# Optimization experiments

Measured on AMD Instinct MI355X. Metric: run time of the kernel, lower is better.

Reference implementation:

```python
import jax, jax.numpy as jnp
import numpy as np

B, N, D = 4, 4096, 512

def setup_inputs() -> dict:
    key = jax.random.key(0)
    ks = jax.random.split(key, 7)
    s = 1.0 / np.sqrt(D)
    return {
        "inputdata": jax.random.normal(ks[0], (B, N, D), dtype=jnp.float32),
        "Wq": jax.random.uniform(ks[1], (D, D), jnp.float32, -s, s),
        "bq": jax.random.uniform(ks[2], (D,), jnp.float32, -s, s),
        "Wk": jax.random.uniform(ks[3], (D, D), jnp.float32, -s, s),
        "bk": jax.random.uniform(ks[4], (D,), jnp.float32, -s, s),
        "Wv": jax.random.uniform(ks[5], (D, D), jnp.float32, -s, s),
        "bv": jax.random.uniform(ks[6], (D,), jnp.float32, -s, s),
    }

def reference(inputdata, Wq, bq, Wk, bk, Wv, bv):
    # torch nn.Linear: y = x @ W^T + b
    Q = jnp.einsum("bnd,ed->bne", inputdata, Wq) + bq  # [B,N,D]
    K = jnp.einsum("bnd,ed->bne", inputdata, Wk) + bk
    V = jnp.einsum("bnd,ed->bne", inputdata, Wv) + bv
    scores = jnp.einsum("bqd,bkd->bqk", Q, K)          # [B,N,N], no 1/sqrt(d) scale
    # NOTE: softmax over dim=1 (the QUERY axis), matching the original torch code
    attn = jax.nn.softmax(scores, axis=1)
    return jnp.einsum("bqk,bkd->bqd", attn, V)         # [B,N,D]
```

## Files before the change

kernel.cpp:

```cpp
#include <hip/hip_runtime.h>
#include <cstdint>


#define NB 4
#define NN 4096
#define ND 512
#define NTOK (NB * NN)

typedef __attribute__((ext_vector_type(8))) short bf16x8;
typedef __attribute__((ext_vector_type(4))) float f32x4;

__device__ __forceinline__ short f2bf(float x) {
  uint32_t u = __float_as_uint(x);
  u += 0x7FFFu + ((u >> 16) & 1u);
  return (short)(u >> 16);
}
__device__ __forceinline__ float bf2f(short h) {
  return __uint_as_float(((uint32_t)(uint16_t)h) << 16);
}
__device__ __forceinline__ void splitf(float x, short& hi, short& lo) {
  short h = f2bf(x);
  hi = h;
  lo = f2bf(x - bf2f(h));
}
__device__ __forceinline__ unsigned int pack2(short a, short b) {
  return (unsigned int)(uint16_t)a | ((unsigned int)(uint16_t)b << 16);
}

__device__ __forceinline__ int xcd_swz(int flat, int nwg) {
  const int cpx = nwg >> 3;
  return (flat & 7) * cpx + (flat >> 3);
}

__device__ __forceinline__ void stage_glds(const short* gbase, long long row_stride,
                                           int row0, int k0, short* ldsplane,
                                           int lane, int wv) {
#pragma unroll
  for (int j = 0; j < 2; ++j) {
    const int chunk = j * 4 + wv;
    const int e = chunk * 512 + lane * 8;
    const int r = e >> 5, k = e & 31;
    const short* src = gbase + (long long)(row0 + r) * row_stride + (k0 + k);
    __builtin_amdgcn_global_load_lds(
        (const __attribute__((address_space(1))) unsigned int*)src,
        (__attribute__((address_space(3))) unsigned int*)(ldsplane + chunk * 512),
        16, 0, 0);
  }
}

__device__ __forceinline__ void mfma_block(const short* lAh, const short* lAl, int astride,
                                           const short* lBh, const short* lBl,
                                           int lane, int wv, f32x4 acc[4][4]) {
  const int ar0 = (wv >> 1) * 64 + (lane & 15);
  const int br0 = (wv & 1) * 64 + (lane & 15);
  const int ko = (lane >> 4) * 8;
  bf16x8 ah[4], al[4], bh[4], bl[4];
#pragma unroll
  for (int f = 0; f < 4; ++f) {
    ah[f] = *(const bf16x8*)(lAh + (ar0 + f * 16) * astride + ko);
    al[f] = *(const bf16x8*)(lAl + (ar0 + f * 16) * astride + ko);
    bh[f] = *(const bf16x8*)(lBh + (br0 + f * 16) * 32 + ko);
    bl[f] = *(const bf16x8*)(lBl + (br0 + f * 16) * 32 + ko);
  }
#pragma unroll
  for (int fm = 0; fm < 4; ++fm)
#pragma unroll
    for (int fn = 0; fn < 4; ++fn)
      acc[fm][fn] = __builtin_amdgcn_mfma_f32_16x16x32_bf16(ah[fm], bh[fn], acc[fm][fn], 0, 0, 0);
#pragma unroll
  for (int fm = 0; fm < 4; ++fm)
#pragma unroll
    for (int fn = 0; fn < 4; ++fn)
      acc[fm][fn] = __builtin_amdgcn_mfma_f32_16x16x32_bf16(ah[fm], bl[fn], acc[fm][fn], 0, 0, 0);
#pragma unroll
  for (int fm = 0; fm < 4; ++fm)
#pragma unroll
    for (int fn = 0; fn < 4; ++fn)
      acc[fm][fn] = __builtin_amdgcn_mfma_f32_16x16x32_bf16(al[fm], bh[fn], acc[fm][fn], 0, 0, 0);
}

__global__ __launch_bounds__(256) void wconv_kernel(
    const float* __restrict__ Wq, const float* __restrict__ Wk, const float* __restrict__ Wv,
    short* __restrict__ Whi, short* __restrict__ Wlo) {
  const int i = blockIdx.x * 256 + threadIdx.x;
  const int m = i >> 16;
  const int e4 = i & 65535;
  const float* W = (m == 0) ? Wq : ((m == 1) ? Wk : Wv);
  const float4 v = ((const float4*)W)[e4];
  short h0, h1, h2, h3, l0, l1, l2, l3;
  splitf(v.x, h0, l0); splitf(v.y, h1, l1); splitf(v.z, h2, l2); splitf(v.w, h3, l3);
  unsigned int* oh = (unsigned int*)(Whi + m * (512 * 512));
  unsigned int* ol = (unsigned int*)(Wlo + m * (512 * 512));
  oh[e4 * 2] = pack2(h0, h1);
  oh[e4 * 2 + 1] = pack2(h2, h3);
  ol[e4 * 2] = pack2(l0, l1);
  ol[e4 * 2 + 1] = pack2(l2, l3);
}

__global__ __launch_bounds__(256, 2) void proj_kernel(
    const float* __restrict__ X, const short* __restrict__ Whi, const short* __restrict__ Wlo,
    const float* __restrict__ bq, const float* __restrict__ bk, const float* __restrict__ bv,
    short* __restrict__ Qhi, short* __restrict__ Qlo,
    short* __restrict__ Khi, short* __restrict__ Klo,
    short* __restrict__ Vthi, short* __restrict__ Vtlo) {
  __shared__ short lAh[128 * 40], lAl[128 * 40];
  __shared__ short lBh[128 * 32], lBl[128 * 32];
  const int tid = threadIdx.x, lane = tid & 63, wv = tid >> 6;
  const int tile = xcd_swz(blockIdx.y * gridDim.x + blockIdx.x, gridDim.x * gridDim.y);
  const int row0 = (tile / 12) * 128;
  const int col0 = (tile % 12) * 128;
  const int mtx = col0 >> 9;
  const int e0 = col0 & 511;
  const short* WhM = Whi + mtx * (512 * 512);
  const short* WlM = Wlo + mtx * (512 * 512);
  f32x4 acc[4][4] = {};
  const int pr = tid >> 1, pc0 = (tid & 1) * 16;
  unsigned int* wAh = (unsigned int*)lAh;
  unsigned int* wAl = (unsigned int*)lAl;

  for (int k0 = 0; k0 < ND; k0 += 32) {
    __syncthreads();
    {
      const float* Xr = X + (long long)(row0 + pr) * ND + k0 + pc0;
      const int wbase = pr * 20 + (pc0 >> 1);
#pragma unroll
      for (int j = 0; j < 4; ++j) {
        const float4 x4 = *(const float4*)(Xr + j * 4);
        short h0, h1, h2, h3, l0, l1, l2, l3;
        splitf(x4.x, h0, l0); splitf(x4.y, h1, l1); splitf(x4.z, h2, l2); splitf(x4.w, h3, l3);
        wAh[wbase + j * 2] = pack2(h0, h1);
        wAh[wbase + j * 2 + 1] = pack2(h2, h3);
        wAl[wbase + j * 2] = pack2(l0, l1);
        wAl[wbase + j * 2 + 1] = pack2(l2, l3);
      }
    }
    stage_glds(WhM, 512, e0, k0, lBh, lane, wv);
    stage_glds(WlM, 512, e0, k0, lBl, lane, wv);
    __syncthreads();
    mfma_block(lAh, lAl, 40, lBh, lBl, lane, wv, acc);
  }

  const float* bias = (mtx == 0) ? bq : ((mtx == 1) ? bk : bv);
  if (mtx < 2) {
    short* Dh = (mtx == 0) ? Qhi : Khi;
    short* Dl = (mtx == 0) ? Qlo : Klo;
    float bb[4];
#pragma unroll
    for (int fn = 0; fn < 4; ++fn)
      bb[fn] = bias[e0 + (wv & 1) * 64 + (lane & 15) + fn * 16];
#pragma unroll
    for (int fm = 0; fm < 4; ++fm) {
      __syncthreads();
#pragma unroll
      for (int fn = 0; fn < 4; ++fn) {
        const int cc = (wv & 1) * 64 + (lane & 15) + fn * 16;
#pragma unroll
        for (int v = 0; v < 4; ++v) {
          const int rs = (wv >> 1) * 16 + ((lane >> 4) << 2) + v;
          short h, l;
          splitf(acc[fm][fn][v] + bb[fn], h, l);
          lAh[rs * 128 + cc] = h;
          lAl[rs * 128 + cc] = l;
        }
      }
      __syncthreads();
#pragma unroll
      for (int s = 0; s < 2; ++s) {
        const int idx = tid + s * 256;
        const int rs = idx >> 4, ch = idx & 15;
        const int gr = row0 + (rs >> 4) * 64 + fm * 16 + (rs & 15);
        const long long o = (long long)gr * ND + e0 + ch * 8;
        *(uint4*)(Dh + o) = *(const uint4*)(lAh + rs * 128 + ch * 8);
        *(uint4*)(Dl + o) = *(const uint4*)(lAl + rs * 128 + ch * 8);
      }
    }
  } else {
    const int lr_base = (wv >> 1) * 64 + ((lane >> 4) << 2);
    const int lc_base = (wv & 1) * 64 + (lane & 15);
#pragma unroll
    for (int fm = 0; fm < 4; ++fm) {
      const int rg = row0 + lr_base + fm * 16;
#pragma unroll
      for (int fn = 0; fn < 4; ++fn) {
        const int e = e0 + lc_base + fn * 16;
        const float bb = bias[e];
        const int b = rg >> 12, n0 = rg & 4095;
        short h0, h1, h2, h3, l0, l1, l2, l3;
        splitf(acc[fm][fn][0] + bb, h0, l0);
        splitf(acc[fm][fn][1] + bb, h1, l1);
        splitf(acc[fm][fn][2] + bb, h2, l2);
        splitf(acc[fm][fn][3] + bb, h3, l3);
        const long long o = ((long long)b * ND + e) * NN + n0;
        *(uint2*)(Vthi + o) = make_uint2(pack2(h0, h1), pack2(h2, h3));
        *(uint2*)(Vtlo + o) = make_uint2(pack2(l0, l1), pack2(l2, l3));
      }
    }
  }
}

__global__ __launch_bounds__(256, 2) void qk_kernel(
    const short* __restrict__ Qh, const short* __restrict__ Ql,
    const short* __restrict__ Kh, const short* __restrict__ Kl,
    short* __restrict__ Ph, short* __restrict__ Pl, float* __restrict__ pl) {
  __shared__ short lAh[128 * 32], lAl[128 * 32], lBh[128 * 32], lBl[128 * 32];
  const int tid = threadIdx.x, lane = tid & 63, wv = tid >> 6;
  const int tile = xcd_swz(blockIdx.y * gridDim.x + blockIdx.x, gridDim.x * gridDim.y);
  const int q0 = (tile / 32) * 128, c0 = (tile % 32) * 128;
  f32x4 acc[4][4] = {};
  for (int k0 = 0; k0 < ND; k0 += 32) {
    __syncthreads();
    stage_glds(Qh, ND, q0, k0, lAh, lane, wv);
    stage_glds(Ql, ND, q0, k0, lAl, lane, wv);
    stage_glds(Kh, ND, c0, k0, lBh, lane, wv);
    stage_glds(Kl, ND, c0, k0, lBl, lane, wv);
    __syncthreads();
    mfma_block(lAh, lAl, 32, lBh, lBl, lane, wv, acc);
  }

#pragma unroll
  for (int fm = 0; fm < 4; ++fm)
#pragma unroll
    for (int fn = 0; fn < 4; ++fn)
#pragma unroll
      for (int v = 0; v < 4; ++v) acc[fm][fn][v] = __expf(acc[fm][fn][v]);

#pragma unroll
  for (int fn = 0; fn < 4; ++fn) {
    float l = 0.f;
#pragma unroll
    for (int fm = 0; fm < 4; ++fm)
#pragma unroll
      for (int v = 0; v < 4; ++v) l += acc[fm][fn][v];
    l += __shfl_xor(l, 16);
    l += __shfl_xor(l, 32);
    if ((lane >> 4) == 0) {
      const long long prow =
          (long long)((q0 >> 7) * 2 + (wv >> 1)) * NN + c0 + (wv & 1) * 64 + lane;
      pl[prow + fn * 16] = l;
    }
  }

#pragma unroll
  for (int fm = 0; fm < 4; ++fm) {
    __syncthreads();
#pragma unroll
    for (int fn = 0; fn < 4; ++fn) {
      const int cc = (wv & 1) * 64 + (lane & 15) + fn * 16;
#pragma unroll
      for (int v = 0; v < 4; ++v) {
        const int rs = (wv >> 1) * 16 + ((lane >> 4) << 2) + v;
        short h, l;
        splitf(acc[fm][fn][v], h, l);
        lAh[rs * 128 + cc] = h;
        lAl[rs * 128 + cc] = l;
      }
    }
    __syncthreads();
#pragma unroll
    for (int s = 0; s < 2; ++s) {
      const int idx = tid + s * 256;
      const int rs = idx >> 4, ch = idx & 15;
      const int gr = q0 + (rs >> 4) * 64 + fm * 16 + (rs & 15);
      const long long o = (long long)gr * NN + c0 + ch * 8;
      *(uint4*)(Ph + o) = *(const uint4*)(lAh + rs * 128 + ch * 8);
      *(uint4*)(Pl + o) = *(const uint4*)(lAl + rs * 128 + ch * 8);
    }
  }
}

__global__ __launch_bounds__(256) void stats_combine_kernel(
    const float* __restrict__ pl, float* __restrict__ Li) {
  const int col = blockIdx.x * 256 + threadIdx.x;
  float l = 0.f;
#pragma unroll 8
  for (int i = 0; i < 64; ++i) l += pl[(long long)i * NN + col];
  Li[col] = 1.0f / l;
}

__global__ __launch_bounds__(256) void vscale_kernel(
    const short* __restrict__ Vth, const short* __restrict__ Vtl,
    const float* __restrict__ Li, short* __restrict__ Vsh, short* __restrict__ Vsl) {
  const int t = blockIdx.x * 256 + threadIdx.x;
  const long long base = (long long)t * 8;
  const int k0 = (int)(base & (NN - 1));
  const uint4 vh = *(const uint4*)(Vth + base);
  const uint4 vl = *(const uint4*)(Vtl + base);
  const float4 li0 = *(const float4*)(Li + k0);
  const float4 li1 = *(const float4*)(Li + k0 + 4);
  const unsigned int* ph = (const unsigned int*)&vh;
  const unsigned int* plo = (const unsigned int*)&vl;
  float li[8] = {li0.x, li0.y, li0.z, li0.w, li1.x, li1.y, li1.z, li1.w};
  short h[8], l[8];
#pragma unroll
  for (int j = 0; j < 8; ++j) {
    const unsigned int wh = ph[j >> 1], wl = plo[j >> 1];
    const short sh = (short)((j & 1) ? (wh >> 16) : wh);
    const short sl = (short)((j & 1) ? (wl >> 16) : wl);
    const float v = (bf2f(sh) + bf2f(sl)) * li[j];
    splitf(v, h[j], l[j]);
  }
  uint4 oh, ol;
  oh.x = pack2(h[0], h[1]); oh.y = pack2(h[2], h[3]);
  oh.z = pack2(h[4], h[5]); oh.w = pack2(h[6], h[7]);
  ol.x = pack2(l[0], l[1]); ol.y = pack2(l[2], l[3]);
  ol.z = pack2(l[4], l[5]); ol.w = pack2(l[6], l[7]);
  *(uint4*)(Vsh + base) = oh;
  *(uint4*)(Vsl + base) = ol;
}

__global__ __launch_bounds__(256, 2) void pv_splitk_kernel(
    const short* __restrict__ Ph, const short* __restrict__ Pl,
    const short* __restrict__ Vh, const short* __restrict__ Vl,
    float* __restrict__ partials) {
  __shared__ short lAh[128 * 32], lAl[128 * 32], lBh[128 * 32], lBl[128 * 32];
  const int tid = threadIdx.x, lane = tid & 63, wv = tid >> 6;
  const int tile = xcd_swz(blockIdx.y * gridDim.x + blockIdx.x, gridDim.x * gridDim.y);
  const int d0 = (tile % 4) * 128, q0 = (tile / 4) * 128;
  const int kb = blockIdx.z * 512;
  f32x4 acc[4][4] = {};
  for (int k0 = kb; k0 < kb + 512; k0 += 32) {
    __syncthreads();
    stage_glds(Ph, NN, q0, k0, lAh, lane, wv);
    stage_glds(Pl, NN, q0, k0, lAl, lane, wv);
    stage_glds(Vh, NN, d0, k0, lBh, lane, wv);
    stage_glds(Vl, NN, d0, k0, lBl, lane, wv);
    __syncthreads();
    mfma_block(lAh, lAl, 32, lBh, lBl, lane, wv, acc);
  }
  const int lr = (wv >> 1) * 64 + ((lane >> 4) << 2);
  const int lc = (wv & 1) * 64 + (lane & 15);
  float* Pd = partials + (long long)blockIdx.z * (NN * ND);
#pragma unroll
  for (int fm = 0; fm < 4; ++fm)
#pragma unroll
    for (int fn = 0; fn < 4; ++fn)
#pragma unroll
      for (int v = 0; v < 4; ++v)
        Pd[(long long)(q0 + lr + fm * 16 + v) * ND + (d0 + lc + fn * 16)] = acc[fm][fn][v];
}

__global__ __launch_bounds__(256) void reduce_kernel(
    const float* __restrict__ partials, float* __restrict__ Ob) {
  const int i = blockIdx.x * 256 + threadIdx.x;
  const float4* p = (const float4*)partials;
  const int stride = (NN * ND) / 4;
  float4 s = p[i];
#pragma unroll
  for (int c = 1; c < 8; ++c) {
    const float4 t = p[i + c * stride];
    s.x += t.x; s.y += t.y; s.z += t.z; s.w += t.w;
  }
  ((float4*)Ob)[i] = s;
}

extern "C" void kernel_launch(void* const* d_in, const int* in_sizes, int n_in,
                              void* d_out, int out_size, void* d_ws, size_t ws_size,
                              hipStream_t stream) {
  (void)in_sizes; (void)n_in; (void)out_size; (void)ws_size;
  const float* X = (const float*)d_in[0];
  const float* Wq = (const float*)d_in[1];
  const float* bq = (const float*)d_in[2];
  const float* Wk = (const float*)d_in[3];
  const float* bk = (const float*)d_in[4];
  const float* Wv = (const float*)d_in[5];
  const float* bv = (const float*)d_in[6];
  float* out = (float*)d_out;

  char* ws = (char*)d_ws;
  size_t off = 0;
  auto take = [&](size_t bytes) -> char* {
    char* p = ws + off;
    off += (bytes + 255) & ~(size_t)255;
    return p;
  };
  short* Qhi = (short*)take((size_t)NTOK * ND * 2);
  short* Qlo = (short*)take((size_t)NTOK * ND * 2);
  short* Khi = (short*)take((size_t)NTOK * ND * 2);
  short* Klo = (short*)take((size_t)NTOK * ND * 2);
  short* Vthi = (short*)take((size_t)NTOK * ND * 2);
  short* Vtlo = (short*)take((size_t)NTOK * ND * 2);
  short* Whi = (short*)take((size_t)3 * 512 * 512 * 2);
  short* Wlo = (short*)take((size_t)3 * 512 * 512 * 2);
  float* Li = (float*)take((size_t)NN * 4);
  float* pl = (float*)take((size_t)64 * NN * 4);
  short* Vshi = (short*)take((size_t)ND * NN * 2);
  short* Vslo = (short*)take((size_t)ND * NN * 2);
  float* S = (float*)take((size_t)NN * NN * 4);
  short* Phi = (short*)take((size_t)NN * NN * 2);
  short* Plo = (short*)take((size_t)NN * NN * 2);

  hipLaunchKernelGGL(wconv_kernel, dim3(768), dim3(256), 0, stream, Wq, Wk, Wv, Whi, Wlo);
  hipLaunchKernelGGL(proj_kernel, dim3(12, 128), dim3(256), 0, stream,
                     X, Whi, Wlo, bq, bk, bv, Qhi, Qlo, Khi, Klo, Vthi, Vtlo);

  for (int b = 0; b < NB; ++b) {
    const long long tb = (long long)b * NN * ND;
    hipLaunchKernelGGL(qk_kernel, dim3(32, 32), dim3(256), 0, stream,
                       Qhi + tb, Qlo + tb, Khi + tb, Klo + tb, Phi, Plo, pl);
    hipLaunchKernelGGL(stats_combine_kernel, dim3(16), dim3(256), 0, stream, pl, Li);
    hipLaunchKernelGGL(vscale_kernel, dim3((ND * NN) / 2048), dim3(256), 0, stream,
                       Vthi + tb, Vtlo + tb, Li, Vshi, Vslo);
    hipLaunchKernelGGL(pv_splitk_kernel, dim3(4, 32, 8), dim3(256), 0, stream,
                       Phi, Plo, Vshi, Vslo, S );
    hipLaunchKernelGGL(reduce_kernel, dim3((NN * ND) / 1024), dim3(256), 0, stream,
                       S , out + tb);
  }
}
```

Measured before the change: 778.1 us.

## Double-buffer QK and PV GEMMs with 8-wave blocks and swizzled LDS

Rewrites the QK and PV split-K GEMM kernels to use 512-thread blocks (8 waves, each owning a 64x32 sub-tile), a 64-wide K step, and double-buffered LDS staging. The next K tile's global-to-LDS loads are issued before the MFMAs on the current tile, so the load latency is hidden behind compute. LDS rows are XOR-swizzled to avoid bank conflicts, and s_setprio is raised around the MFMA bursts. LDS use grows to 128 KB per block, which may limit occupancy to one block per CU despite the launch bound.

```diff
diff --git a/kernel.cpp b/kernel.cpp
--- a/kernel.cpp
+++ b/kernel.cpp
@@ -77,6 +77,72 @@
 #pragma unroll
     for (int fn = 0; fn < 4; ++fn)
       acc[fm][fn] = __builtin_amdgcn_mfma_f32_16x16x32_bf16(al[fm], bh[fn], acc[fm][fn], 0, 0, 0);
+}
+
+__device__ __forceinline__ void stage8(const short* gA_h, const short* gA_l,
+                                       const short* gB_h, const short* gB_l,
+                                       long long strideA, long long strideB,
+                                       int rowA0, int rowB0, int k0,
+                                       short* ldsbuf, int lane, int wid) {
+  const int plane = wid >> 1, h = wid & 1;
+  const short* g = (plane == 0) ? gA_h : (plane == 1) ? gA_l : (plane == 2) ? gB_h : gB_l;
+  const long long stride = (plane < 2) ? strideA : strideB;
+  const int row0 = ((plane < 2) ? rowA0 : rowB0) + h * 64;
+  short* lp = ldsbuf + plane * 8192 + h * 64 * 64;
+  const int rsub = lane >> 3;
+  const int csub = ((lane & 7) ^ rsub) * 8;
+#pragma unroll
+  for (int c = 0; c < 8; ++c) {
+    const short* src = g + (long long)(row0 + c * 8 + rsub) * stride + (k0 + csub);
+    __builtin_amdgcn_global_load_lds(
+        (const __attribute__((address_space(1))) unsigned int*)src,
+        (__attribute__((address_space(3))) unsigned int*)(lp + c * 512),
+        16, 0, 0);
+  }
+}
+
+__device__ __forceinline__ void mfma_tile8(const short* base, int lane, int wr, int wc,
+                                           f32x4 acc[4][2]) {
+  const int al = lane & 15, lg = lane >> 4;
+  const short* pAh = base;
+  const short* pAl = base + 8192;
+  const short* pBh = base + 16384;
+  const short* pBl = base + 24576;
+#pragma unroll
+  for (int ksub = 0; ksub < 2; ++ksub) {
+    bf16x8 ah[4], alo[4], bh[2], bl[2];
+#pragma unroll
+    for (int fm = 0; fm < 4; ++fm) {
+      const int row = wr * 64 + fm * 16 + al;
+      const int slot = (ksub * 4 + lg) ^ (row & 7);
+      ah[fm] = *(const bf16x8*)(pAh + row * 64 + slot * 8);
+      alo[fm] = *(const bf16x8*)(pAl + row * 64 + slot * 8);
+    }
+#pragma unroll
+    for (int fn = 0; fn < 2; ++fn) {
+      const int row = wc * 32 + fn * 16 + al;
+      const int slot = (ksub * 4 + lg) ^ (row & 7);
+      bh[fn] = *(const bf16x8*)(pBh + row * 64 + slot * 8);
+      bl[fn] = *(const bf16x8*)(pBl + row * 64 + slot * 8);
+    }
+    __builtin_amdgcn_s_setprio(1);
+#pragma unroll
+    for (int fm = 0; fm < 4; ++fm)
+#pragma unroll
+      for (int fn = 0; fn < 2; ++fn)
+        acc[fm][fn] = __builtin_amdgcn_mfma_f32_16x16x32_bf16(ah[fm], bh[fn], acc[fm][fn], 0, 0, 0);
+#pragma unroll
+    for (int fm = 0; fm < 4; ++fm)
+#pragma unroll
+      for (int fn = 0; fn < 2; ++fn)
+        acc[fm][fn] = __builtin_amdgcn_mfma_f32_16x16x32_bf16(ah[fm], bl[fn], acc[fm][fn], 0, 0, 0);
+#pragma unroll
+    for (int fm = 0; fm < 4; ++fm)
+#pragma unroll
+      for (int fn = 0; fn < 2; ++fn)
+        acc[fm][fn] = __builtin_amdgcn_mfma_f32_16x16x32_bf16(alo[fm], bh[fn], acc[fm][fn], 0, 0, 0);
+    __builtin_amdgcn_s_setprio(0);
+  }
 }
 
 __global__ __launch_bounds__(256) void wconv_kernel(
@@ -198,34 +264,40 @@
   }
 }
 
-__global__ __launch_bounds__(256, 2) void qk_kernel(
+__global__ __launch_bounds__(512, 2) void qk8_kernel(
     const short* __restrict__ Qh, const short* __restrict__ Ql,
     const short* __restrict__ Kh, const short* __restrict__ Kl,
     short* __restrict__ Ph, short* __restrict__ Pl, float* __restrict__ pl) {
-  __shared__ short lAh[128 * 32], lAl[128 * 32], lBh[128 * 32], lBl[128 * 32];
-  const int tid = threadIdx.x, lane = tid & 63, wv = tid >> 6;
+  __shared__ short lds[2][4][8192];
+  const int tid = threadIdx.x, lane = tid & 63, wid = tid >> 6;
+  const int wr = wid >> 2, wc = wid & 3;
+  const int al = lane & 15, lg = lane >> 4;
   const int tile = xcd_swz(blockIdx.y * gridDim.x + blockIdx.x, gridDim.x * gridDim.y);
   const int q0 = (tile / 32) * 128, c0 = (tile % 32) * 128;
-  f32x4 acc[4][4] = {};
-  for (int k0 = 0; k0 < ND; k0 += 32) {
+  f32x4 acc[4][2] = {};
+
+  stage8(Qh, Ql, Kh, Kl, ND, ND, q0, c0, 0, &lds[0][0][0], lane, wid);
+  asm volatile("s_waitcnt vmcnt(0)" ::: "memory");
+  __syncthreads();
+
+  for (int kt = 0; kt < 8; ++kt) {
+    const int cur = kt & 1;
+    if (kt < 7)
+      stage8(Qh, Ql, Kh, Kl, ND, ND, q0, c0, (kt + 1) * 64, &lds[cur ^ 1][0][0], lane, wid);
+    mfma_tile8(&lds[cur][0][0], lane, wr, wc, acc);
+    asm volatile("s_waitcnt vmcnt(0)" ::: "memory");
     __syncthreads();
-    stage_glds(Qh, ND, q0, k0, lAh, lane, wv);
-    stage_glds(Ql, ND, q0, k0, lAl, lane, wv);
-    stage_glds(Kh, ND, c0, k0, lBh, lane, wv);
-    stage_glds(Kl, ND, c0, k0, lBl, lane, wv);
-    __syncthreads();
-    mfma_block(lAh, lAl, 32, lBh, lBl, lane, wv, acc);
-  }
-
-#pragma unroll
-  for (int fm = 0; fm < 4; ++fm)
-#pragma unroll
-    for (int fn = 0; fn < 4; ++fn)
+  }
+
+#pragma unroll
+  for (int fm = 0; fm < 4; ++fm)
+#pragma unroll
+    for (int fn = 0; fn < 2; ++fn)
 #pragma unroll
       for (int v = 0; v < 4; ++v) acc[fm][fn][v] = __expf(acc[fm][fn][v]);
 
 #pragma unroll
-  for (int fn = 0; fn < 4; ++fn) {
+  for (int fn = 0; fn < 2; ++fn) {
     float l = 0.f;
 #pragma unroll
     for (int fm = 0; fm < 4; ++fm)
@@ -233,38 +305,37 @@
       for (int v = 0; v < 4; ++v) l += acc[fm][fn][v];
     l += __shfl_xor(l, 16);
     l += __shfl_xor(l, 32);
-    if ((lane >> 4) == 0) {
+    if (lg == 0) {
       const long long prow =
-          (long long)((q0 >> 7) * 2 + (wv >> 1)) * NN + c0 + (wv & 1) * 64 + lane;
-      pl[prow + fn * 16] = l;
-    }
-  }
-
-#pragma unroll
-  for (int fm = 0; fm < 4; ++fm) {
-    __syncthreads();
-#pragma unroll
-    for (int fn = 0; fn < 4; ++fn) {
-      const int cc = (wv & 1) * 64 + (lane & 15) + fn * 16;
+          (long long)((q0 >> 7) * 2 + wr) * NN + c0 + wc * 32 + fn * 16 + al;
+      pl[prow] = l;
+    }
+  }
+
+  short* th = &lds[0][0][0];
+  short* tl = &lds[0][2][0];
+  __syncthreads();
+#pragma unroll
+  for (int fm = 0; fm < 4; ++fm)
+#pragma unroll
+    for (int fn = 0; fn < 2; ++fn)
 #pragma unroll
       for (int v = 0; v < 4; ++v) {
-        const int rs = (wv >> 1) * 16 + ((lane >> 4) << 2) + v;
+        const int row = wr * 64 + fm * 16 + lg * 4 + v;
+        const int col = wc * 32 + fn * 16 + al;
         short h, l;
         splitf(acc[fm][fn][v], h, l);
-        lAh[rs * 128 + cc] = h;
-        lAl[rs * 128 + cc] = l;
-      }
-    }
-    __syncthreads();
-#pragma unroll
-    for (int s = 0; s < 2; ++s) {
-      const int idx = tid + s * 256;
-      const int rs = idx >> 4, ch = idx & 15;
-      const int gr = q0 + (rs >> 4) * 64 + fm * 16 + (rs & 15);
-      const long long o = (long long)gr * NN + c0 + ch * 8;
-      *(uint4*)(Ph + o) = *(const uint4*)(lAh + rs * 128 + ch * 8);
-      *(uint4*)(Pl + o) = *(const uint4*)(lAl + rs * 128 + ch * 8);
-    }
+        th[row * 128 + col] = h;
+        tl[row * 128 + col] = l;
+      }
+  __syncthreads();
+#pragma unroll
+  for (int s = 0; s < 4; ++s) {
+    const int idx = tid + s * 512;
+    const int rs = idx >> 4, ch = idx & 15;
+    const long long o = (long long)(q0 + rs) * NN + c0 + ch * 8;
+    *(uint4*)(Ph + o) = *(const uint4*)(th + rs * 128 + ch * 8);
+    *(uint4*)(Pl + o) = *(const uint4*)(tl + rs * 128 + ch * 8);
   }
 }
 
@@ -308,35 +379,43 @@
   *(uint4*)(Vsl + base) = ol;
 }
 
-__global__ __launch_bounds__(256, 2) void pv_splitk_kernel(
+__global__ __launch_bounds__(512, 2) void pv8_kernel(
     const short* __restrict__ Ph, const short* __restrict__ Pl,
     const short* __restrict__ Vh, const short* __restrict__ Vl,
     float* __restrict__ partials) {
-  __shared__ short lAh[128 * 32], lAl[128 * 32], lBh[128 * 32], lBl[128 * 32];
-  const int tid = threadIdx.x, lane = tid & 63, wv = tid >> 6;
+  __shared__ short lds[2][4][8192];
+  const int tid = threadIdx.x, lane = tid & 63, wid = tid >> 6;
+  const int wr = wid >> 2, wc = wid & 3;
+  const int al = lane & 15, lg = lane >> 4;
   const int tile = xcd_swz(blockIdx.y * gridDim.x + blockIdx.x, gridDim.x * gridDim.y);
   const int d0 = (tile % 4) * 128, q0 = (tile / 4) * 128;
   const int kb = blockIdx.z * 512;
-  f32x4 acc[4][4] = {};
-  for (int k0 = kb; k0 < kb + 512; k0 += 32) {
+  f32x4 acc[4][2] = {};
+
+  stage8(Ph, Pl, Vh, Vl, NN, NN, q0, d0, kb, &lds[0][0][0], lane, wid);
+  asm volatile("s_waitcnt vmcnt(0)" ::: "memory");
+  __syncthreads();
+
+  for (int kt = 0; kt < 8; ++kt) {
+    const int cur = kt & 1;
+    if (kt < 7)
+      stage8(Ph, Pl, Vh, Vl, NN, NN, q0, d0, kb + (kt + 1) * 64, &lds[cur ^ 1][0][0], lane, wid);
+    mfma_tile8(&lds[cur][0][0], lane, wr, wc, acc);
+    asm volatile("s_waitcnt vmcnt(0)" ::: "memory");
     __syncthreads();
-    stage_glds(Ph, NN, q0, k0, lAh, lane, wv);
-    stage_glds(Pl, NN, q0, k0, lAl, lane, wv);
-    stage_glds(Vh, NN, d0, k0, lBh, lane, wv);
-    stage_glds(Vl, NN, d0, k0, lBl, lane, wv);
-    __syncthreads();
-    mfma_block(lAh, lAl, 32, lBh, lBl, lane, wv, acc);
-  }
-  const int lr = (wv >> 1) * 64 + ((lane >> 4) << 2);
-  const int lc = (wv & 1) * 64 + (lane & 15);
+  }
+
   float* Pd = partials + (long long)blockIdx.z * (NN * ND);
 #pragma unroll
   for (int fm = 0; fm < 4; ++fm)
 #pragma unroll
-    for (int fn = 0; fn < 4; ++fn)
-#pragma unroll
-      for (int v = 0; v < 4; ++v)
-        Pd[(long long)(q0 + lr + fm * 16 + v) * ND + (d0 + lc + fn * 16)] = acc[fm][fn][v];
+    for (int fn = 0; fn < 2; ++fn)
+#pragma unroll
+      for (int v = 0; v < 4; ++v) {
+        const int row = q0 + wr * 64 + fm * 16 + lg * 4 + v;
+        const int col = d0 + wc * 32 + fn * 16 + al;
+        Pd[(long long)row * ND + col] = acc[fm][fn][v];
+      }
 }
 
 __global__ __launch_bounds__(256) void reduce_kernel(
@@ -395,12 +474,12 @@
 
   for (int b = 0; b < NB; ++b) {
     const long long tb = (long long)b * NN * ND;
-    hipLaunchKernelGGL(qk_kernel, dim3(32, 32), dim3(256), 0, stream,
+    hipLaunchKernelGGL(qk8_kernel, dim3(32, 32), dim3(512), 0, stream,
                        Qhi + tb, Qlo + tb, Khi + tb, Klo + tb, Phi, Plo, pl);
     hipLaunchKernelGGL(stats_combine_kernel, dim3(16), dim3(256), 0, stream, pl, Li);
     hipLaunchKernelGGL(vscale_kernel, dim3((ND * NN) / 2048), dim3(256), 0, stream,
                        Vthi + tb, Vtlo + tb, Li, Vshi, Vslo);
-    hipLaunchKernelGGL(pv_splitk_kernel, dim3(4, 32, 8), dim3(256), 0, stream,
+    hipLaunchKernelGGL(pv8_kernel, dim3(4, 32, 8), dim3(512), 0, stream,
                        Phi, Plo, Vshi, Vslo, S );
     hipLaunchKernelGGL(reduce_kernel, dim3((NN * ND) / 1024), dim3(256), 0, stream,
                        S , out + tb);
```

Result: no change. 769.0 us (-1.2%).
